# Kernel tuning notes

Hardware: AMD Instinct MI355X
Metric: run time of the kernel (lower is better)

## Reference

```python
import jax, jax.numpy as jnp
import numpy as np

B, L, D, H, P, NL, TOPK = 2, 512, 512, 16, 128, 2, 3
DH = D // H
FF = 4 * D
EPS = 1e-5
NEG = -1e9


def _ln(h):
    mu = jnp.mean(h, axis=-1, keepdims=True)
    var = jnp.mean((h - mu) ** 2, axis=-1, keepdims=True)
    return (h - mu) * jax.lax.rsqrt(var + EPS)


def setup_inputs() -> dict:
    key = jax.random.key(0)
    ks = jax.random.split(key, 16)
    def nrm(k, shape, s=0.02):
        return jax.random.normal(k, shape, dtype=jnp.float32) * s
    lengths = jax.random.randint(ks[0], (B,), L // 2, L + 1)
    padding_mask = jnp.arange(L)[None, :] >= lengths[:, None]  # [B,L] bool, True = pad
    return {
        'x': jax.random.normal(ks[1], (L, B, D), dtype=jnp.float32),
        'pos': jax.random.normal(ks[2], (B, L, 3), dtype=jnp.float32),
        'time_emb': jax.random.normal(ks[3], (B, 1, D), dtype=jnp.float32),
        'pair_feat': jax.random.normal(ks[4], (B, L, L, P), dtype=jnp.float32),
        'pos_emb_w': nrm(ks[5], (D, 3), 0.1),
        'pfb_w': nrm(ks[6], (H, P), 0.1),
        'p2n_w1': nrm(ks[7], (P, P)),
        'p2n_w2': nrm(ks[8], (D, P)),
        'adaln_w': nrm(ks[9], (NL, 6 * D, D)),
        'adaln_b': jnp.zeros((NL, 6 * D), jnp.float32),
        'qkv_w': nrm(ks[10], (NL, 3 * D, D)),
        'qkv_b': jnp.zeros((NL, 3 * D), jnp.float32),
        'proj_w': nrm(ks[11], (NL, D, D)),
        'proj_b': jnp.zeros((NL, D), jnp.float32),
        'mlp_w1': nrm(ks[12], (NL, FF, D)),
        'mlp_b1': jnp.zeros((NL, FF), jnp.float32),
        'mlp_w2': nrm(ks[13], (NL, D, FF)),
        'mlp_b2': jnp.zeros((NL, D), jnp.float32),
        'padding_mask': padding_mask,
    }


def _forward(x, pos, time_emb, pair_feat, pos_emb_w, pfb_w, p2n_w1, p2n_w2,
             adaln_w, adaln_b, qkv_w, qkv_b, proj_w, proj_b,
             mlp_w1, mlp_b1, mlp_w2, mlp_b2, padding_mask):
    x = jnp.swapaxes(x, 0, 1)  # [B,L,D]
    keep = (~padding_mask).astype(x.dtype)  # [B,L]
    pos_embedding = (pos @ pos_emb_w.T) * keep[..., None]  # [B,L,D], masked_fill(pad,0)
    # pair bias: SiLU -> Linear(P,H), then permute to [B,H,L,L]
    pfb = jnp.einsum('blmp,hp->bhlm', jax.nn.silu(pair_feat), pfb_w)
    # mask pair features on both residue axes
    pf = pair_feat * keep[:, None, :, None] * keep[:, :, None, None]  # [B,L,L,P]
    # topk over dim=1 (rows) per (b, col): transpose so rows are last axis
    col_scores = jnp.swapaxes(jnp.mean(pfb, axis=1), 1, 2)  # [B, L(col), L(row)]
    _, idx = jax.lax.top_k(col_scores, TOPK)  # [B, L, K]
    idx = jnp.moveaxis(idx, 2, 1)  # [B, K, L]
    f2n = jnp.mean(jnp.take_along_axis(pf, idx[..., None], axis=1), axis=1)  # [B,L,P]
    f2n = jax.nn.silu(f2n @ p2n_w1.T) @ p2n_w2.T  # pair2node MLP -> [B,L,D]
    x = x + f2n  # condition stream
    cond = jax.nn.silu(x)
    scale = 1.0 / np.sqrt(DH)
    h = pos_embedding
    for l in range(NL):  # DiT blocks (adaLN modulation from cond, MHA with pair bias, GELU MLP)
        hin = h + time_emb
        mod = cond @ adaln_w[l].T + adaln_b[l]  # [B,L,6D]
        sh_a, sc_a, g_a, sh_m, sc_m, g_m = jnp.split(mod, 6, axis=-1)
        a = _ln(hin) * (1.0 + sc_a) + sh_a
        q, k, v = jnp.split(a @ qkv_w[l].T + qkv_b[l], 3, axis=-1)
        q = q.reshape(B, L, H, DH)
        k = k.reshape(B, L, H, DH)
        v = v.reshape(B, L, H, DH)
        s = jnp.einsum('blhd,bmhd->bhlm', q, k) * scale + pfb
        s = jnp.where(padding_mask[:, None, None, :], NEG, s)
        o = jnp.einsum('bhlm,bmhd->blhd', jax.nn.softmax(s, axis=-1), v).reshape(B, L, D)
        hin = hin + g_a * (o @ proj_w[l].T + proj_b[l])
        m = _ln(hin) * (1.0 + sc_m) + sh_m
        m = jax.nn.gelu(m @ mlp_w1[l].T + mlp_b1[l]) @ mlp_w2[l].T + mlp_b2[l]
        h = hin + g_m * m
    return h  # [B,L,D]


def reference(x, pos, time_emb, pair_feat, pos_emb_w, pfb_w, p2n_w1, p2n_w2,
              adaln_w, adaln_b, qkv_w, qkv_b, proj_w, proj_b,
              mlp_w1, mlp_b1, mlp_w2, mlp_b2, padding_mask):
    return _forward(x, pos, time_emb, pair_feat, pos_emb_w, pfb_w, p2n_w1, p2n_w2,
                    adaln_w, adaln_b, qkv_w, qkv_b, proj_w, proj_b,
                    mlp_w1, mlp_b1, mlp_w2, mlp_b2, padding_mask)
```

## Files before the change

### kernel.cpp

```cpp
#include <hip/hip_runtime.h>
#include <hip/hip_bf16.h>
#include <math.h>

#define B_  2
#define L_  512
#define D_  512
#define H_  16
#define P_  128
#define NL_ 2
#define DH_ 32
#define FF_ 2048
#define NT_ (B_*L_)

typedef __bf16 bf16_t;
typedef bf16_t bf16x8 __attribute__((ext_vector_type(8)));
typedef bf16_t bf16x4 __attribute__((ext_vector_type(4)));
typedef bf16_t bf16x2 __attribute__((ext_vector_type(2)));
typedef float  f32x4  __attribute__((ext_vector_type(4)));

__device__ __forceinline__ float siluf(float x){ return x / (1.f + __expf(-x)); }
__device__ __forceinline__ float geluf(float x){
  const float c = 0.7978845608028654f;
  float x3 = x*x*x;
  return 0.5f*x*(1.f + tanhf(c*(x + 0.044715f*x3)));
}

__device__ __forceinline__ void gload16(const bf16_t* g, bf16_t* l){
  __builtin_amdgcn_global_load_lds(
      (const __attribute__((address_space(1))) unsigned int*)g,
      (__attribute__((address_space(3))) unsigned int*)l, 16, 0, 0);
}

#define NB_CVT 9216
#define NB_POS 1024
__global__ __launch_bounds__(256) void k_pre(
      const float* __restrict__ s0, const float* __restrict__ s1,
      const float* __restrict__ s2, const float* __restrict__ s3,
      const float* __restrict__ s4, bf16_t* __restrict__ wdst,
      const float* __restrict__ pos, const float* __restrict__ posw,
      const int* __restrict__ maskp, float* __restrict__ h, float* __restrict__ keepf,
      const float* __restrict__ pair, const float* __restrict__ pfw,
      bf16_t* __restrict__ pfb, float* __restrict__ colm){
  __shared__ float sw[16][128];
  int bid = blockIdx.x;
  int tid = threadIdx.x;
  if (bid < NB_CVT){
    const size_t c0=3145728, c1=4718592, c2=5242880, c3=7340032, c4=9437184;
    size_t e = ((size_t)bid*256 + tid)*4;
    if (e >= c4) return;
    const float* s; size_t off;
    if      (e < c0){ s=s0; off=e; }
    else if (e < c1){ s=s1; off=e-c0; }
    else if (e < c2){ s=s2; off=e-c1; }
    else if (e < c3){ s=s3; off=e-c2; }
    else            { s=s4; off=e-c3; }
    float4 v = *(const float4*)(s + off);
    bf16x4 o; o[0]=(bf16_t)v.x; o[1]=(bf16_t)v.y; o[2]=(bf16_t)v.z; o[3]=(bf16_t)v.w;
    *(bf16x4*)(wdst + e) = o;
    return;
  }
  if (bid < NB_CVT + NB_POS){
    int n = bid - NB_CVT;
    float kf = (maskp[n] != 0) ? 0.f : 1.f;
    if (tid == 0) keepf[n] = kf;
    float p0 = pos[n*3+0], p1 = pos[n*3+1], p2 = pos[n*3+2];
    for (int d = tid; d < D_; d += 256){
      float v = p0*posw[d*3+0] + p1*posw[d*3+1] + p2*posw[d*3+2];
      h[(size_t)n*D_ + d] = kf*v;
    }
    return;
  }
  int blk = bid - NB_CVT - NB_POS;
  int mc = blk & 1;
  int n  = blk >> 1;
  int b = n >> 9, l = n & 511;
  {
    float4* swv = (float4*)&sw[0][0];
    const float4* wv = (const float4*)pfw;
    swv[tid] = wv[tid];
    swv[tid + 256] = wv[tid + 256];
  }
  __syncthreads();
  int m = mc*256 + tid;
  const float* rowp = pair + (((size_t)n)*512 + m)*128;
  float acc[16] = {};
  #pragma unroll 4
  for (int pc = 0; pc < 32; ++pc){
    float4 v = ((const float4*)rowp)[pc];
    v.x = siluf(v.x); v.y = siluf(v.y); v.z = siluf(v.z); v.w = siluf(v.w);
    #pragma unroll
    for (int hh = 0; hh < 16; ++hh){
      float4 wv = *(const float4*)&sw[hh][pc*4];
      acc[hh] += v.x*wv.x + v.y*wv.y + v.z*wv.z + v.w*wv.w;
    }
  }
  float mean = 0.f;
  #pragma unroll
  for (int hh = 0; hh < 16; ++hh) mean += acc[hh];
  colm[((size_t)n)*512 + m] = mean * (1.f/16.f);
  #pragma unroll
  for (int hh = 0; hh < 16; ++hh)
    pfb[(((size_t)(b*16 + hh))*512 + l)*512 + m] = (bf16_t)acc[hh];
}

__global__ __launch_bounds__(128) void k_topk_f2n(const float* __restrict__ colm,
      const float* __restrict__ pair, const float* __restrict__ keepf,
      const float* __restrict__ w1, const float* __restrict__ w2,
      const float* __restrict__ xin, bf16_t* __restrict__ cond){
  int n = blockIdx.x; int b = n >> 9, m = n & 511;
  __shared__ int sidx[3];
  __shared__ float f2n_s[128];
  __shared__ float u_s[128];
  int tid = threadIdx.x;
  if (tid < 64){
    const float* colbase = colm + ((size_t)b*512)*512 + m;
    float v[8];
    #pragma unroll
    for (int i = 0; i < 8; ++i) v[i] = colbase[(size_t)(tid + 64*i)*512];
    int c0 = -1, c1 = -1;
    for (int r = 0; r < 3; ++r){
      float bv = -INFINITY; int bi = 1 << 30;
      #pragma unroll
      for (int i = 0; i < 8; ++i){
        int idx = tid + 64*i;
        bool excl = (idx == c0) || (idx == c1);
        float val = v[i];
        if (!excl && (val > bv || (val == bv && idx < bi))){ bv = val; bi = idx; }
      }
      for (int o = 32; o > 0; o >>= 1){
        float ov = __shfl_down(bv, o);
        int   oi = __shfl_down(bi, o);
        if (ov > bv || (ov == bv && oi < bi)){ bv = ov; bi = oi; }
      }
      bi = __shfl(bi, 0);
      if (tid == 0) sidx[r] = bi;
      if (r == 0) c0 = bi; else c1 = bi;
    }
  }
  __syncthreads();
  int i0 = sidx[0], i1 = sidx[1], i2 = sidx[2];
  float kc = keepf[n];
  float k0 = keepf[b*512 + i0], k1 = keepf[b*512 + i1], k2 = keepf[b*512 + i2];
  {
    int p = tid;
    float s = k0*pair[(((size_t)(b*512 + i0))*512 + m)*128 + p]
            + k1*pair[(((size_t)(b*512 + i1))*512 + m)*128 + p]
            + k2*pair[(((size_t)(b*512 + i2))*512 + m)*128 + p];
    f2n_s[p] = s * kc * (1.f/3.f);
  }
  __syncthreads();
  {
    int j = tid;
    const float* wr = w1 + (size_t)j*128;
    float acc = 0.f;
    #pragma unroll 8
    for (int p = 0; p < 128; ++p) acc += f2n_s[p]*wr[p];
    u_s[j] = siluf(acc);
  }
  __syncthreads();
  for (int d = tid; d < 512; d += 128){
    const float* wr = w2 + (size_t)d*128;
    float acc = 0.f;
    #pragma unroll 8
    for (int p = 0; p < 128; ++p) acc += u_s[p]*wr[p];
    float xv = xin[((size_t)(m*2 + b))*512 + d];
    cond[(size_t)n*512 + d] = (bf16_t)siluf(xv + acc);
  }
}

__global__ __launch_bounds__(128) void k_lnmod2(const float* __restrict__ hbase,
      const float* __restrict__ te, const bf16_t* __restrict__ mod,
      bf16_t* __restrict__ out, int sh_off, int sc_off, int mstride){
  int n = blockIdx.x; int b = n >> 9;
  int tid = threadIdx.x;
  float4 v = ((const float4*)(hbase + (size_t)n*512))[tid];
  if (te){
    float4 t = ((const float4*)(te + (size_t)b*512))[tid];
    v.x += t.x; v.y += t.y; v.z += t.z; v.w += t.w;
  }
  float s = v.x + v.y + v.z + v.w;
  float q = v.x*v.x + v.y*v.y + v.z*v.z + v.w*v.w;
  #pragma unroll
  for (int o = 1; o < 64; o <<= 1){ s += __shfl_xor(s, o); q += __shfl_xor(q, o); }
  __shared__ float s2[2], q2[2];
  if ((tid & 63) == 0){ s2[tid >> 6] = s; q2[tid >> 6] = q; }
  __syncthreads();
  float S = s2[0] + s2[1], Q = q2[0] + q2[1];
  float mean = S * (1.f/512.f);
  float var  = Q * (1.f/512.f) - mean*mean;
  float rstd = rsqrtf(var + 1e-5f);
  const bf16_t* mrow = mod + (size_t)n*mstride;
  bf16x4 sc = *(const bf16x4*)(mrow + sc_off + tid*4);
  bf16x4 sh = *(const bf16x4*)(mrow + sh_off + tid*4);
  bf16x4 rv;
  rv[0] = (bf16_t)((v.x - mean)*rstd*(1.f + (float)sc[0]) + (float)sh[0]);
  rv[1] = (bf16_t)((v.y - mean)*rstd*(1.f + (float)sc[1]) + (float)sh[1]);
  rv[2] = (bf16_t)((v.z - mean)*rstd*(1.f + (float)sc[2]) + (float)sh[2]);
  rv[3] = (bf16_t)((v.w - mean)*rstd*(1.f + (float)sc[3]) + (float)sh[3]);
  *(bf16x4*)(out + (size_t)n*512 + tid*4) = rv;
}

template<int BM, int BN>
__global__ __launch_bounds__(256) void k_gemm_bf(const bf16_t* __restrict__ A,
      const bf16_t* __restrict__ Bw, const float* __restrict__ bias,
      int M, int N, int K, int epi,
      float* __restrict__ outf, bf16_t* __restrict__ outb,
      const float* __restrict__ res, const bf16_t* __restrict__ gate, int gate_ld,
      const float* __restrict__ te, bf16_t* __restrict__ vT){
  const int FM = BM/32, FN = BN/32;
  const int CA = BM/32, CB = BN/32;
  __shared__ __align__(16) bf16_t As[2][BM*64];
  __shared__ __align__(16) bf16_t Bs[2][BN*64];
  int tid = threadIdx.x;
  int m0 = blockIdx.y*BM, n0 = blockIdx.x*BN;
  int lane = tid & 63, wid = tid >> 6;
  int wr = wid >> 1, wc = wid & 1;
  int frow = lane & 15, g = lane >> 4;
  f32x4 acc[FM][FN] = {};

  auto stage = [&](int buf, int k0){
    int e = tid;
    #pragma unroll
    for (int i = 0; i < CA; ++i, e += 256){
      int row = e >> 3, cb = e & 7;
      gload16(A + (size_t)(m0+row)*K + k0 + ((cb ^ (row&7))<<3), &As[buf][e*8]);
    }
    e = tid;
    #pragma unroll
    for (int i = 0; i < CB; ++i, e += 256){
      int row = e >> 3, cb = e & 7;
      gload16(Bw + (size_t)(n0+row)*K + k0 + ((cb ^ (row&7))<<3), &Bs[buf][e*8]);
    }
  };
  auto compute = [&](int buf){
    #pragma unroll
    for (int ks = 0; ks < 2; ++ks){
      bf16x8 af[FM], bfv[FN];
      #pragma unroll
      for (int fm = 0; fm < FM; ++fm){
        int ar = wr*(BM/2) + fm*16 + frow;
        af[fm] = *(const bf16x8*)&As[buf][ar*64 + (((ks*4+g) ^ (ar&7))<<3)];
      }
      #pragma unroll
      for (int fn = 0; fn < FN; ++fn){
        int br = wc*(BN/2) + fn*16 + frow;
        bfv[fn] = *(const bf16x8*)&Bs[buf][br*64 + (((ks*4+g) ^ (br&7))<<3)];
      }
      #pragma unroll
      for (int fm = 0; fm < FM; ++fm)
        #pragma unroll
        for (int fn = 0; fn < FN; ++fn)
          acc[fm][fn] = __builtin_amdgcn_mfma_f32_16x16x32_bf16(af[fm], bfv[fn], acc[fm][fn], 0,0,0);
    }
  };

  stage(0, 0);
  __syncthreads();
  int cur = 0;
  for (int k0 = 64; k0 < K; k0 += 64){
    stage(cur^1, k0);
    compute(cur);
    __syncthreads();
    cur ^= 1;
  }
  compute(cur);

  #pragma unroll
  for (int fm = 0; fm < FM; ++fm){
    #pragma unroll
    for (int fn = 0; fn < FN; ++fn){
      int n = n0 + wc*(BN/2) + fn*16 + frow;
      float bb = bias[n];
      int row0 = m0 + wr*(BM/2) + fm*16 + g*4;
      if (epi == 3 && n >= 1024){
        int hh = (n-1024)>>5, dh = (n-1024)&31;
        int b = row0>>9, ll = row0&511;
        bf16x4 pv;
        #pragma unroll
        for (int i = 0; i < 4; ++i){
          float v = acc[fm][fn][i] + bb;
          outb[(size_t)(row0+i)*N + n] = (bf16_t)v;
          pv[i] = (bf16_t)v;
        }
        *(bf16x4*)&vT[(((size_t)(b*16+hh))*32 + dh)*512 + ll] = pv;
      } else {
        #pragma unroll
        for (int i = 0; i < 4; ++i){
          int row = row0 + i;
          float v = acc[fm][fn][i] + bb;
          if (epi == 1){
            v = res[(size_t)row*N + n] + te[(row>>9)*D_ + n]
              + (float)gate[(size_t)row*gate_ld + n]*v;
            outf[(size_t)row*N + n] = v;
          } else if (epi == 2){
            outb[(size_t)row*N + n] = (bf16_t)geluf(v);
          } else if (epi == 3){
            outb[(size_t)row*N + n] = (bf16_t)v;
          } else if (epi == 4){
            v = res[(size_t)row*N + n] + (float)gate[(size_t)row*gate_ld + n]*v;
            outf[(size_t)row*N + n] = v;
          } else {
            outb[(size_t)row*N + n] = (bf16_t)v;
          }
        }
      }
    }
  }
}

__global__ __launch_bounds__(256) void k_attn2(const bf16_t* __restrict__ qkv,
      const bf16_t* __restrict__ vT, const bf16_t* __restrict__ pfb,
      const float* __restrict__ keepf, bf16_t* __restrict__ obuf){
  __shared__ float ss[16][516];
  __shared__ float opart[4][16][33];
  __shared__ float inv_s[16];
  int blk = blockIdx.x;
  int qt = blk & 31;
  int bh = blk >> 5;
  int b = bh >> 4, h = bh & 15;
  int r0 = qt*16;
  int tid = threadIdx.x;
  int lane = tid & 63, w = tid >> 6;
  int frow = lane & 15, g = lane >> 4;
  const float scale = 0.17677669529663687f;
  bf16x8 qf = *(const bf16x8*)(qkv + (size_t)(b*512 + r0 + frow)*1536 + h*32 + g*8);
  bf16x8 kf[8];
  #pragma unroll
  for (int t = 0; t < 8; ++t){
    int kc = w*128 + t*16;
    kf[t] = *(const bf16x8*)(qkv + (size_t)(b*512 + kc + frow)*1536 + 512 + h*32 + g*8);
  }
  #pragma unroll
  for (int t = 0; t < 8; ++t){
    int kc = w*128 + t*16;
    f32x4 s4 = {};
    s4 = __builtin_amdgcn_mfma_f32_16x16x32_bf16(kf[t], qf, s4, 0,0,0);
    int tok0 = kc + g*4;
    float4 kp = *(const float4*)&keepf[b*512 + tok0];
    bf16x4 pb = *(const bf16x4*)&pfb[((size_t)bh*512 + r0 + frow)*512 + tok0];
    float4 sv;
    sv.x = (kp.x == 0.f) ? -1e9f : s4[0]*scale + (float)pb[0];
    sv.y = (kp.y == 0.f) ? -1e9f : s4[1]*scale + (float)pb[1];
    sv.z = (kp.z == 0.f) ? -1e9f : s4[2]*scale + (float)pb[2];
    sv.w = (kp.w == 0.f) ? -1e9f : s4[3]*scale + (float)pb[3];
    *(float4*)&ss[frow][tok0] = sv;
  }
  bf16x8 vf[4][2];
  #pragma unroll
  for (int t = 0; t < 4; ++t){
    int kc = w*128 + t*32;
    #pragma unroll
    for (int fn = 0; fn < 2; ++fn)
      vf[t][fn] = *(const bf16x8*)(vT + ((size_t)bh*32 + fn*16 + frow)*512 + kc + g*8);
  }
  __syncthreads();
  {
    int r = tid >> 4, mo = tid & 15;
    float mx = -INFINITY;
    #pragma unroll 8
    for (int t2 = 0; t2 < 32; ++t2) mx = fmaxf(mx, ss[r][mo + 16*t2]);
    #pragma unroll
    for (int o = 1; o < 16; o <<= 1) mx = fmaxf(mx, __shfl_xor(mx, o));
    float sum = 0.f;
    #pragma unroll 8
    for (int t2 = 0; t2 < 32; ++t2){
      int m = mo + 16*t2;
      float e = __expf(ss[r][m] - mx);
      ss[r][m] = e;
      sum += e;
    }
    #pragma unroll
    for (int o = 1; o < 16; o <<= 1) sum += __shfl_xor(sum, o);
    if (mo == 0) inv_s[r] = 1.f/sum;
  }
  __syncthreads();
  f32x4 oacc[2] = {};
  #pragma unroll
  for (int t = 0; t < 4; ++t){
    int kc = w*128 + t*32;
    float4 p0 = *(const float4*)&ss[frow][kc + g*8];
    float4 p1 = *(const float4*)&ss[frow][kc + g*8 + 4];
    bf16x8 pfr;
    pfr[0]=(bf16_t)p0.x; pfr[1]=(bf16_t)p0.y; pfr[2]=(bf16_t)p0.z; pfr[3]=(bf16_t)p0.w;
    pfr[4]=(bf16_t)p1.x; pfr[5]=(bf16_t)p1.y; pfr[6]=(bf16_t)p1.z; pfr[7]=(bf16_t)p1.w;
    #pragma unroll
    for (int fn = 0; fn < 2; ++fn)
      oacc[fn] = __builtin_amdgcn_mfma_f32_16x16x32_bf16(pfr, vf[t][fn], oacc[fn], 0,0,0);
  }
  #pragma unroll
  for (int fn = 0; fn < 2; ++fn)
    #pragma unroll
    for (int i = 0; i < 4; ++i)
      opart[w][g*4+i][fn*16+frow] = oacc[fn][i];
  __syncthreads();
  {
    int q = tid >> 4, dh = (tid & 15)*2;
    float o0 = 0.f, o1 = 0.f;
    #pragma unroll
    for (int ww = 0; ww < 4; ++ww){ o0 += opart[ww][q][dh]; o1 += opart[ww][q][dh+1]; }
    float inv = inv_s[q];
    bf16x2 ov; ov[0] = (bf16_t)(o0*inv); ov[1] = (bf16_t)(o1*inv);
    *(bf16x2*)(obuf + (size_t)(b*512 + r0 + q)*512 + h*32 + dh) = ov;
  }
}

extern "C" void kernel_launch(void* const* d_in, const int* in_sizes, int n_in,
                              void* d_out, int out_size, void* d_ws, size_t ws_size,
                              hipStream_t stream){
  (void)in_sizes; (void)n_in; (void)out_size; (void)ws_size;
  const float* x        = (const float*)d_in[0];
  const float* pos      = (const float*)d_in[1];
  const float* time_emb = (const float*)d_in[2];
  const float* pair     = (const float*)d_in[3];
  const float* pos_w    = (const float*)d_in[4];
  const float* pfb_w    = (const float*)d_in[5];
  const float* p2n_w1   = (const float*)d_in[6];
  const float* p2n_w2   = (const float*)d_in[7];
  const float* adaln_w  = (const float*)d_in[8];
  const float* adaln_b  = (const float*)d_in[9];
  const float* qkv_w    = (const float*)d_in[10];
  const float* qkv_b    = (const float*)d_in[11];
  const float* proj_w   = (const float*)d_in[12];
  const float* proj_b   = (const float*)d_in[13];
  const float* mlp_w1   = (const float*)d_in[14];
  const float* mlp_b1   = (const float*)d_in[15];
  const float* mlp_w2   = (const float*)d_in[16];
  const float* mlp_b2   = (const float*)d_in[17];
  const int*   maskp    = (const int*)d_in[18];

  float* W = (float*)d_ws;
  size_t off = 0;
  auto alloc = [&](size_t nfw){ float* p = W + off; off += nfw; return p; };
  float*  h     = alloc(524288);
  float*  hin2  = alloc(524288);
  bf16_t* modb  = (bf16_t*)alloc(3145728);
  float*  colm  = alloc(524288);
  float*  keepf = alloc(1024);
  bf16_t* pfbb  = (bf16_t*)alloc(4194304);
  bf16_t* condb = (bf16_t*)alloc(262144);
  bf16_t* abuf  = (bf16_t*)alloc(262144);
  bf16_t* qkvb  = (bf16_t*)alloc(786432);
  bf16_t* vTb   = (bf16_t*)alloc(262144);
  bf16_t* midb  = (bf16_t*)alloc(1048576);
  bf16_t* obuf  = (bf16_t*)alloc(262144);
  bf16_t* wB    = (bf16_t*)alloc(4718592);
  bf16_t* wA  = wB;
  bf16_t* wQ  = wB + 3145728;
  bf16_t* wP  = wB + 4718592;
  bf16_t* wM1 = wB + 5242880;
  bf16_t* wM2 = wB + 7340032;

  k_pre<<<NB_CVT + NB_POS + NT_*2, 256, 0, stream>>>(
      adaln_w, qkv_w, proj_w, mlp_w1, mlp_w2, wB,
      pos, pos_w, maskp, h, keepf,
      pair, pfb_w, pfbb, colm);
  k_topk_f2n<<<NT_, 128, 0, stream>>>(colm, pair, keepf, p2n_w1, p2n_w2, x, condb);
  k_gemm_bf<64,64><<<dim3(96,16), 256, 0, stream>>>(condb, wA, adaln_b,
      NT_, 6144, 512, 0, nullptr, modb, nullptr, nullptr, 0, nullptr, nullptr);

  for (int l = 0; l < NL_; ++l){
    const bf16_t* modl = modb + (size_t)l*3072;
    k_lnmod2<<<NT_, 128, 0, stream>>>(h, time_emb, modl, abuf, 0, 512, 6144);
    k_gemm_bf<64,64><<<dim3(24,16), 256, 0, stream>>>(abuf, wQ + (size_t)l*1536*512,
        qkv_b + (size_t)l*1536, NT_, 1536, 512, 3, nullptr, qkvb, nullptr, nullptr, 0, nullptr, vTb);
    k_attn2<<<B_*H_*32, 256, 0, stream>>>(qkvb, vTb, pfbb, keepf, obuf);
    k_gemm_bf<64,32><<<dim3(16,16), 256, 0, stream>>>(obuf, wP + (size_t)l*512*512,
        proj_b + (size_t)l*512, NT_, 512, 512, 1, hin2, nullptr, h,
        modl + 2*512, 6144, time_emb, nullptr);
    k_lnmod2<<<NT_, 128, 0, stream>>>(hin2, nullptr, modl, abuf, 3*512, 4*512, 6144);
    k_gemm_bf<64,64><<<dim3(32,16), 256, 0, stream>>>(abuf, wM1 + (size_t)l*2048*512,
        mlp_b1 + (size_t)l*2048, NT_, 2048, 512, 2, nullptr, midb, nullptr, nullptr, 0, nullptr, nullptr);
    float* hout = (l == NL_-1) ? (float*)d_out : h;
    k_gemm_bf<64,32><<<dim3(16,16), 256, 0, stream>>>(midb, wM2 + (size_t)l*512*2048,
        mlp_b2 + (size_t)l*512, NT_, 512, 2048, 4, hout, nullptr, hin2,
        modl + 5*512, 6144, nullptr, nullptr);
  }
}
```

Measured before the change: 336.4 us.

## Triple-buffer GEMM LDS staging with vmcnt-based waits; vectorize pair-to-node matvecs

The bf16 MFMA GEMM moves from a double-buffered LDS pipeline to a three-stage ring. It prefetches two K-tiles ahead and uses explicit s_waitcnt vmcnt counts plus raw s_barrier instead of __syncthreads. The aim is to keep more global-to-LDS loads in flight and hide memory latency behind MFMA work. The small pair-to-node MLP loops also switch to float4 loads. The cost is 1.5x the shared memory, which can lower occupancy. The tail iterations wait with a nonzero vmcnt even when no newer stage was issued, so the last tile may be read before its loads finish.

```diff
diff --git a/kernel.cpp b/kernel.cpp
--- a/kernel.cpp
+++ b/kernel.cpp
@@ -29,6 +29,13 @@
   __builtin_amdgcn_global_load_lds(
       (const __attribute__((address_space(1))) unsigned int*)g,
       (__attribute__((address_space(3))) unsigned int*)l, 16, 0, 0);
+}
+
+template<int N> __device__ __forceinline__ void wait_vm(){
+  if constexpr (N == 3)      asm volatile("s_waitcnt vmcnt(3)" ::: "memory");
+  else if constexpr (N == 4) asm volatile("s_waitcnt vmcnt(4)" ::: "memory");
+  else if constexpr (N == 6) asm volatile("s_waitcnt vmcnt(6)" ::: "memory");
+  else                       asm volatile("s_waitcnt vmcnt(0)" ::: "memory");
 }
 
 #define NB_CVT 9216
@@ -151,18 +158,26 @@
   __syncthreads();
   {
     int j = tid;
-    const float* wr = w1 + (size_t)j*128;
+    const float4* wr4 = (const float4*)(w1 + (size_t)j*128);
     float acc = 0.f;
     #pragma unroll 8
-    for (int p = 0; p < 128; ++p) acc += f2n_s[p]*wr[p];
+    for (int pc = 0; pc < 32; ++pc){
+      float4 wv = wr4[pc];
+      float4 fv = *(const float4*)&f2n_s[pc*4];
+      acc += fv.x*wv.x + fv.y*wv.y + fv.z*wv.z + fv.w*wv.w;
+    }
     u_s[j] = siluf(acc);
   }
   __syncthreads();
   for (int d = tid; d < 512; d += 128){
-    const float* wr = w2 + (size_t)d*128;
+    const float4* wr4 = (const float4*)(w2 + (size_t)d*128);
     float acc = 0.f;
     #pragma unroll 8
-    for (int p = 0; p < 128; ++p) acc += u_s[p]*wr[p];
+    for (int pc = 0; pc < 32; ++pc){
+      float4 wv = wr4[pc];
+      float4 uv = *(const float4*)&u_s[pc*4];
+      acc += uv.x*wv.x + uv.y*wv.y + uv.z*wv.z + uv.w*wv.w;
+    }
     float xv = xin[((size_t)(m*2 + b))*512 + d];
     cond[(size_t)n*512 + d] = (bf16_t)siluf(xv + acc);
   }
@@ -209,8 +224,9 @@
       const float* __restrict__ te, bf16_t* __restrict__ vT){
   const int FM = BM/32, FN = BN/32;
   const int CA = BM/32, CB = BN/32;
-  __shared__ __align__(16) bf16_t As[2][BM*64];
-  __shared__ __align__(16) bf16_t Bs[2][BN*64];
+  const int LPS = CA + CB;
+  __shared__ __align__(16) bf16_t As[3*BM*64];
+  __shared__ __align__(16) bf16_t Bs[3*BN*64];
   int tid = threadIdx.x;
   int m0 = blockIdx.y*BM, n0 = blockIdx.x*BN;
   int lane = tid & 63, wid = tid >> 6;
@@ -223,13 +239,13 @@
     #pragma unroll
     for (int i = 0; i < CA; ++i, e += 256){
       int row = e >> 3, cb = e & 7;
-      gload16(A + (size_t)(m0+row)*K + k0 + ((cb ^ (row&7))<<3), &As[buf][e*8]);
+      gload16(A + (size_t)(m0+row)*K + k0 + ((cb ^ (row&7))<<3), &As[buf*BM*64 + e*8]);
     }
     e = tid;
     #pragma unroll
     for (int i = 0; i < CB; ++i, e += 256){
       int row = e >> 3, cb = e & 7;
-      gload16(Bw + (size_t)(n0+row)*K + k0 + ((cb ^ (row&7))<<3), &Bs[buf][e*8]);
+      gload16(Bw + (size_t)(n0+row)*K + k0 + ((cb ^ (row&7))<<3), &Bs[buf*BN*64 + e*8]);
     }
   };
   auto compute = [&](int buf){
@@ -239,12 +255,12 @@
       #pragma unroll
       for (int fm = 0; fm < FM; ++fm){
         int ar = wr*(BM/2) + fm*16 + frow;
-        af[fm] = *(const bf16x8*)&As[buf][ar*64 + (((ks*4+g) ^ (ar&7))<<3)];
+        af[fm] = *(const bf16x8*)&As[buf*BM*64 + ar*64 + (((ks*4+g) ^ (ar&7))<<3)];
       }
       #pragma unroll
       for (int fn = 0; fn < FN; ++fn){
         int br = wc*(BN/2) + fn*16 + frow;
-        bfv[fn] = *(const bf16x8*)&Bs[buf][br*64 + (((ks*4+g) ^ (br&7))<<3)];
+        bfv[fn] = *(const bf16x8*)&Bs[buf*BN*64 + br*64 + (((ks*4+g) ^ (br&7))<<3)];
       }
       #pragma unroll
       for (int fm = 0; fm < FM; ++fm)
@@ -254,16 +270,22 @@
     }
   };
 
+  int nst = K >> 6;
   stage(0, 0);
-  __syncthreads();
-  int cur = 0;
-  for (int k0 = 64; k0 < K; k0 += 64){
-    stage(cur^1, k0);
-    compute(cur);
-    __syncthreads();
-    cur ^= 1;
-  }
-  compute(cur);
+  if (nst > 1) stage(1, 64);
+  wait_vm<LPS>();
+  __builtin_amdgcn_sched_barrier(0);
+  __builtin_amdgcn_s_barrier();
+  __builtin_amdgcn_sched_barrier(0);
+  for (int k = 0; k < nst; ++k){
+    if (k + 2 < nst) stage((k+2)%3, (k+2)*64);
+    compute(k%3);
+    asm volatile("s_waitcnt lgkmcnt(0)" ::: "memory");
+    wait_vm<LPS>();
+    __builtin_amdgcn_sched_barrier(0);
+    __builtin_amdgcn_s_barrier();
+    __builtin_amdgcn_sched_barrier(0);
+  }
 
   #pragma unroll
   for (int fm = 0; fm < FM; ++fm){
```

Result: no change. 332.6 us (-1.1%).
